# Kernel tuning notes

Hardware: AMD Instinct MI355X
Metric: run time of the kernel (lower is better)

The kernel has to match this reference:

```python
import jax, jax.numpy as jnp
import numpy as np

B, N, D, H = 2, 2048, 2048, 16
HD = D // H  # 128


def _rope(x, freqs):
    # x: [b,h,n,d]; freqs: [n, d//2] angles. Interleaved complex rotation.
    cos = jnp.cos(freqs)  # [n, d/2]
    sin = jnp.sin(freqs)
    x2 = x.reshape(*x.shape[:-1], -1, 2)  # [b,h,n,d/2,2]
    xr, xi = x2[..., 0], x2[..., 1]
    out_r = xr * cos - xi * sin
    out_i = xr * sin + xi * cos
    return jnp.stack([out_r, out_i], axis=-1).reshape(x.shape)


def setup_inputs() -> dict:
    key = jax.random.key(0)
    ks = jax.random.split(key, 4)
    x = jax.random.normal(ks[0], (B, N, D), jnp.float32)
    # rotary angle tables: pos * inv_freq, shape [N, HD/2]
    pos = jnp.arange(N, dtype=jnp.float32)
    inv_freq = 1.0 / (10000.0 ** (jnp.arange(0, HD, 2, dtype=jnp.float32) / HD))
    freqs = pos[:, None] * inv_freq[None, :]
    expanded_attn_masks = jnp.ones((B, 1, 1, N), jnp.int32)
    casual_mask = jnp.tril(jnp.ones((N, N), jnp.int32))[None, None]  # [1,1,N,N]
    Wqkv = jax.random.normal(ks[1], (D, 3 * D), jnp.float32) * 0.02
    bqkv = jnp.zeros((3 * D,), jnp.float32)
    Wout = jax.random.normal(ks[2], (D, D), jnp.float32) * 0.02
    bout = jnp.zeros((D,), jnp.float32)
    return {
        'x': x, 'freq_cis_q': freqs, 'freq_cis_k': freqs,
        'expanded_attn_masks': expanded_attn_masks, 'casual_mask': casual_mask,
        'Wqkv': Wqkv, 'bqkv': bqkv, 'Wout': Wout, 'bout': bout,
    }


def reference(x, freq_cis_q, freq_cis_k, expanded_attn_masks, casual_mask, Wqkv, bqkv, Wout, bout):
    b, n, d = x.shape
    qkv = x @ Wqkv + bqkv                                   # [b,n,3d]
    qkv = qkv.reshape(b, n, 3, H, HD)
    qkv = jnp.transpose(qkv, (2, 0, 3, 1, 4))               # c b h n d
    q, k, v = qkv[0], qkv[1], qkv[2]
    next_prefix_kv = jnp.stack((k, v))                      # pre-RoPE k cached, per source
    q = _rope(q, freq_cis_q)
    k = _rope(k, freq_cis_k)
    scores = jnp.einsum('bhqd,bhkd->bhqk', q, k) / jnp.sqrt(jnp.float32(HD))
    mask_value = -jnp.finfo(scores.dtype).max
    scores = jnp.where(casual_mask == 0, mask_value, scores)
    scores = jnp.where(expanded_attn_masks == 0, mask_value, scores)
    p = jax.nn.softmax(scores, axis=-1)                     # dropout_prob=0 -> identity
    attn_o = jnp.einsum('bhqk,bhkd->bhqd', p, v)
    attn_o = jnp.transpose(attn_o, (0, 2, 1, 3)).reshape(b, n, d)
    out = attn_o @ Wout + bout
    return out, next_prefix_kv
```

## Files before the change

kernel.cpp:

```cpp
#include <hip/hip_runtime.h>
#include <hip/hip_bf16.h>
#include <math.h>

#define B_ 2
#define N_ 2048
#define D_ 2048
#define H_ 16
#define HD_ 128
#define D3_ 6144

typedef __attribute__((ext_vector_type(8))) short bf16x8;
typedef __attribute__((ext_vector_type(4))) float f32x4;

__device__ __forceinline__ void gl_lds16(const void* g, void* l) {
  __builtin_amdgcn_global_load_lds(
      (const __attribute__((address_space(1))) void*)g,
      (__attribute__((address_space(3))) void*)l, 16, 0, 0);
}

__device__ __forceinline__ float bf2f(short s) {
  union { float f; unsigned u; } cv;
  cv.u = ((unsigned)(unsigned short)s) << 16;
  return cv.f;
}
__device__ __forceinline__ short f2bf(float f) {
  union { float f; unsigned u; } cv; cv.f = f;
  unsigned u = cv.u;
  unsigned r = (u + 0x7fffu + ((u >> 16) & 1u)) >> 16;
  return (short)r;
}

__global__ void k_cvt_x(const float* __restrict__ x, short* __restrict__ xb, int n) {
  int i = (blockIdx.x * 256 + threadIdx.x) * 4;
  if (i < n) {
    float4 v = *(const float4*)(x + i);
    short4 o;
    o.x = f2bf(v.x); o.y = f2bf(v.y); o.z = f2bf(v.z); o.w = f2bf(v.w);
    *(short4*)(xb + i) = o;
  }
}

__global__ void k_transcvt(const float* __restrict__ in, short* __restrict__ out, int R, int C) {
  __shared__ float t[64][65];
  int r0 = blockIdx.y * 64, c0 = blockIdx.x * 64;
  #pragma unroll
  for (int e0 = 0; e0 < 16; e0++) {
    int e = e0 * 256 + threadIdx.x;
    int r = e >> 6, c = e & 63;
    t[r][c] = in[(long)(r0 + r) * C + c0 + c];
  }
  __syncthreads();
  #pragma unroll
  for (int e0 = 0; e0 < 16; e0++) {
    int e = e0 * 256 + threadIdx.x;
    int c = e >> 6, r = e & 63;
    out[(long)(c0 + c) * R + r0 + r] = f2bf(t[r][c]);
  }
}

__global__ __launch_bounds__(256) void k_gemm(
    const short* __restrict__ A, const short* __restrict__ BT,
    const float* __restrict__ bias, int M, int Nn, int K, int mode,
    short* __restrict__ outb, float* __restrict__ outf, float* __restrict__ kvout)
{
  __shared__ __align__(16) short As[128 * 32];
  __shared__ __align__(16) short Bs[128 * 32];
  int wave = threadIdx.x >> 6, lane = threadIdx.x & 63;
  int quad = lane >> 4, l15 = lane & 15;
  int m0 = blockIdx.y * 128, n0 = blockIdx.x * 128;
  int wm = wave >> 1, wn = wave & 1;
  f32x4 acc[4][4] = {};

  for (int k0 = 0; k0 < K; k0 += 32) {
    const short* gaa = A + (long)(m0 + wave * 32 + (lane >> 2)) * K + k0 + (lane & 3) * 8;
    gl_lds16(gaa,           As + (wave * 32) * 32);
    gl_lds16(gaa + 16 * K,  As + (wave * 32 + 16) * 32);
    const short* gbb = BT + (long)(n0 + wave * 32 + (lane >> 2)) * K + k0 + (lane & 3) * 8;
    gl_lds16(gbb,           Bs + (wave * 32) * 32);
    gl_lds16(gbb + 16 * K,  Bs + (wave * 32 + 16) * 32);
    __syncthreads();
    bf16x8 af[4], bfr[4];
    #pragma unroll
    for (int mi = 0; mi < 4; mi++)
      af[mi] = *(const bf16x8*)(As + (wm * 64 + mi * 16 + l15) * 32 + quad * 8);
    #pragma unroll
    for (int ni = 0; ni < 4; ni++)
      bfr[ni] = *(const bf16x8*)(Bs + (wn * 64 + ni * 16 + l15) * 32 + quad * 8);
    #pragma unroll
    for (int mi = 0; mi < 4; mi++)
      #pragma unroll
      for (int ni = 0; ni < 4; ni++)
        acc[mi][ni] = __builtin_amdgcn_mfma_f32_16x16x32_bf16(af[mi], bfr[ni], acc[mi][ni], 0, 0, 0);
    __syncthreads();
  }

  int row_base = m0 + wm * 64;
  int col_base = n0 + wn * 64;
  #pragma unroll
  for (int mi = 0; mi < 4; mi++) {
    #pragma unroll
    for (int ni = 0; ni < 4; ni++) {
      int col = col_base + ni * 16 + l15;
      float bv = bias[col];
      #pragma unroll
      for (int reg = 0; reg < 4; reg++) {
        int row = row_base + mi * 16 + quad * 4 + reg;
        float v = acc[mi][ni][reg] + bv;
        if (mode == 0) {
          outf[(long)row * Nn + col] = v;
        } else {
          outb[(long)row * Nn + col] = f2bf(v);
          if (col >= D_) {
            int sel = (col >= 2 * D_) ? 1 : 0;
            int c2 = col - D_ - sel * D_;
            int h = c2 >> 7, d = c2 & 127;
            int b = row >> 11, n = row & 2047;
            kvout[((((long)sel * B_ + b) * H_ + h) * N_ + n) * HD_ + d] = v;
          }
        }
      }
    }
  }
}

__global__ void k_rope(const short* __restrict__ qkvb, const float* __restrict__ fq,
                       const float* __restrict__ fk, short* __restrict__ qr,
                       short* __restrict__ kr)
{
  int t = blockIdx.x * 256 + threadIdx.x;
  int i = t & 63;
  int n = (t >> 6) & (N_ - 1);
  int bh = t >> 17;
  int b = bh >> 4, h = bh & 15;
  long qrow = ((long)b * N_ + n) * D3_;
  float q0 = bf2f(qkvb[qrow + h * 128 + 2 * i]);
  float q1 = bf2f(qkvb[qrow + h * 128 + 2 * i + 1]);
  float k0 = bf2f(qkvb[qrow + D_ + h * 128 + 2 * i]);
  float k1 = bf2f(qkvb[qrow + D_ + h * 128 + 2 * i + 1]);
  float aq = fq[n * 64 + i], ak = fk[n * 64 + i];
  float cq, sq, ck, sk;
  __sincosf(aq, &sq, &cq);
  __sincosf(ak, &sk, &ck);
  const float qs = 0.08838834764831845f;
  long orow = ((long)bh * N_ + n) * HD_;
  qr[orow + 2 * i]     = f2bf((q0 * cq - q1 * sq) * qs);
  qr[orow + 2 * i + 1] = f2bf((q0 * sq + q1 * cq) * qs);
  kr[orow + 2 * i]     = f2bf(k0 * ck - k1 * sk);
  kr[orow + 2 * i + 1] = f2bf(k0 * sk + k1 * ck);
}

__global__ void k_vtrans(const short* __restrict__ qkvb, short* __restrict__ vt) {
  __shared__ short t[64][130];
  int nt = blockIdx.x & 31;
  int h = (blockIdx.x >> 5) & 15;
  int b = blockIdx.x >> 9;
  int n0 = nt * 64;
  #pragma unroll
  for (int e0 = 0; e0 < 32; e0++) {
    int e = e0 * 256 + threadIdx.x;
    int r = e >> 7, d = e & 127;
    t[r][d] = qkvb[((long)b * N_ + n0 + r) * D3_ + 2 * D_ + h * 128 + d];
  }
  __syncthreads();
  #pragma unroll
  for (int e0 = 0; e0 < 32; e0++) {
    int e = e0 * 256 + threadIdx.x;
    int d = e >> 6, r = e & 63;
    vt[(((long)(b * H_ + h)) * HD_ + d) * N_ + n0 + r] = t[r][d];
  }
}

__global__ __launch_bounds__(256) void k_flash(
    const short* __restrict__ qr, const short* __restrict__ kr,
    const short* __restrict__ vt, const int* __restrict__ amask,
    short* __restrict__ ao)
{
  __shared__ __align__(16) short Qs[64 * 128];
  __shared__ __align__(16) short Ks[64 * 128];
  __shared__ __align__(16) short Vs[128 * 64];
  __shared__ __align__(16) short Ps[4][16 * 64];
  int qt = blockIdx.x & 31, h = (blockIdx.x >> 5) & 15, b = blockIdx.x >> 9;
  int wave = threadIdx.x >> 6, lane = threadIdx.x & 63;
  int quad = lane >> 4, l15 = lane & 15;
  int q0 = qt * 64;
  long bh = (long)b * H_ + h;

  #pragma unroll
  for (int c = 0; c < 4; c++) {
    const short* g = qr + (bh * N_ + q0 + wave * 16 + c * 4 + (lane >> 4)) * HD_ + l15 * 8;
    gl_lds16(g, Qs + (wave * 16 + c * 4) * 128);
  }
  __syncthreads();
  bf16x8 aq[4];
  #pragma unroll
  for (int kt = 0; kt < 4; kt++)
    aq[kt] = *(const bf16x8*)(Qs + (wave * 16 + l15) * 128 + kt * 32 + quad * 8);

  f32x4 o[8] = {};
  float mrow[4] = {-3e38f, -3e38f, -3e38f, -3e38f};
  float lrow[4] = {0.f, 0.f, 0.f, 0.f};
  int rowq[4];
  #pragma unroll
  for (int reg = 0; reg < 4; reg++) rowq[reg] = q0 + wave * 16 + quad * 4 + reg;

  for (int kvt = 0; kvt <= qt; kvt++) {
    int kv0 = kvt * 64;
    __syncthreads();
    #pragma unroll
    for (int c = 0; c < 4; c++) {
      const short* g = kr + (bh * N_ + kv0 + wave * 16 + c * 4 + (lane >> 4)) * HD_ + l15 * 8;
      gl_lds16(g, Ks + (wave * 16 + c * 4) * 128);
    }
    #pragma unroll
    for (int c = 0; c < 4; c++) {
      const short* g = vt + (bh * HD_ + wave * 32 + c * 8 + (lane >> 3)) * N_ + kv0 + (lane & 7) * 8;
      gl_lds16(g, Vs + (wave * 32 + c * 8) * 64);
    }
    __syncthreads();

    f32x4 s[4] = {};
    #pragma unroll
    for (int kt = 0; kt < 4; kt++) {
      #pragma unroll
      for (int nt = 0; nt < 4; nt++) {
        bf16x8 bk = *(const bf16x8*)(Ks + (nt * 16 + l15) * 128 + kt * 32 + quad * 8);
        s[nt] = __builtin_amdgcn_mfma_f32_16x16x32_bf16(aq[kt], bk, s[nt], 0, 0, 0);
      }
    }
    #pragma unroll
    for (int nt = 0; nt < 4; nt++) {
      int col = kv0 + nt * 16 + l15;
      bool cm = (amask[b * N_ + col] == 0);
      #pragma unroll
      for (int reg = 0; reg < 4; reg++) {
        if (cm || col > rowq[reg]) s[nt][reg] = -3e38f;
      }
    }
    float mn[4], alpha[4];
    #pragma unroll
    for (int reg = 0; reg < 4; reg++) {
      float pm = fmaxf(fmaxf(s[0][reg], s[1][reg]), fmaxf(s[2][reg], s[3][reg]));
      #pragma unroll
      for (int x = 1; x < 16; x <<= 1) pm = fmaxf(pm, __shfl_xor(pm, x, 64));
      mn[reg] = fmaxf(mrow[reg], pm);
      alpha[reg] = __expf(mrow[reg] - mn[reg]);
      mrow[reg] = mn[reg];
    }
    float rs[4] = {0.f, 0.f, 0.f, 0.f};
    #pragma unroll
    for (int nt = 0; nt < 4; nt++)
      #pragma unroll
      for (int reg = 0; reg < 4; reg++) {
        float p = __expf(s[nt][reg] - mn[reg]);
        s[nt][reg] = p;
        rs[reg] += p;
      }
    #pragma unroll
    for (int reg = 0; reg < 4; reg++) {
      #pragma unroll
      for (int x = 1; x < 16; x <<= 1) rs[reg] += __shfl_xor(rs[reg], x, 64);
      lrow[reg] = lrow[reg] * alpha[reg] + rs[reg];
    }
    short* pw = Ps[wave];
    #pragma unroll
    for (int nt = 0; nt < 4; nt++)
      #pragma unroll
      for (int reg = 0; reg < 4; reg++)
        pw[(quad * 4 + reg) * 64 + nt * 16 + l15] = f2bf(s[nt][reg]);
    #pragma unroll
    for (int nt2 = 0; nt2 < 8; nt2++)
      #pragma unroll
      for (int reg = 0; reg < 4; reg++)
        o[nt2][reg] *= alpha[reg];
    asm volatile("s_waitcnt lgkmcnt(0)" ::: "memory");
    #pragma unroll
    for (int kt2 = 0; kt2 < 2; kt2++) {
      bf16x8 ap = *(const bf16x8*)(pw + l15 * 64 + kt2 * 32 + quad * 8);
      #pragma unroll
      for (int nt2 = 0; nt2 < 8; nt2++) {
        bf16x8 bv = *(const bf16x8*)(Vs + (nt2 * 16 + l15) * 64 + kt2 * 32 + quad * 8);
        o[nt2] = __builtin_amdgcn_mfma_f32_16x16x32_bf16(ap, bv, o[nt2], 0, 0, 0);
      }
    }
  }

  #pragma unroll
  for (int reg = 0; reg < 4; reg++) lrow[reg] = 1.0f / lrow[reg];
  #pragma unroll
  for (int nt2 = 0; nt2 < 8; nt2++)
    #pragma unroll
    for (int reg = 0; reg < 4; reg++) {
      int n = q0 + wave * 16 + quad * 4 + reg;
      int d = h * 128 + nt2 * 16 + l15;
      ao[((long)b * N_ + n) * D_ + d] = f2bf(o[nt2][reg] * lrow[reg]);
    }
}

extern "C" void kernel_launch(void* const* d_in, const int* in_sizes, int n_in,
                              void* d_out, int out_size, void* d_ws, size_t ws_size,
                              hipStream_t stream) {
  const float* x    = (const float*)d_in[0];
  const float* fq   = (const float*)d_in[1];
  const float* fk   = (const float*)d_in[2];
  const int*   am   = (const int*)d_in[3];
  const float* Wqkv = (const float*)d_in[5];
  const float* bqkv = (const float*)d_in[6];
  const float* Wout = (const float*)d_in[7];
  const float* bout = (const float*)d_in[8];

  float* out = (float*)d_out;
  float* kvout = out + (long)B_ * N_ * D_;

  char* ws = (char*)d_ws;
  const size_t need = 167772160;
  if (ws_size < need) return;
  short* xb    = (short*)(ws);
  short* wqkvT = (short*)(ws + 16777216);
  short* woutT = (short*)(ws + 41943040);
  short* qkvb  = (short*)(ws + 50331648);
  short* qrb   = (short*)(ws + 100663296);
  short* krb   = (short*)(ws + 117440512);
  short* vtb   = (short*)(ws + 134217728);
  short* aob   = (short*)(ws + 150994944);

  k_cvt_x<<<8192, 256, 0, stream>>>(x, xb, B_ * N_ * D_);
  k_transcvt<<<dim3(D3_ / 64, D_ / 64), 256, 0, stream>>>(Wqkv, wqkvT, D_, D3_);
  k_transcvt<<<dim3(D_ / 64, D_ / 64), 256, 0, stream>>>(Wout, woutT, D_, D_);
  k_gemm<<<dim3(D3_ / 128, (B_ * N_) / 128), 256, 0, stream>>>(
      xb, wqkvT, bqkv, B_ * N_, D3_, D_, 1, qkvb, nullptr, kvout);
  k_rope<<<16384, 256, 0, stream>>>(qkvb, fq, fk, qrb, krb);
  k_vtrans<<<1024, 256, 0, stream>>>(qkvb, vtb);
  k_flash<<<1024, 256, 0, stream>>>(qrb, krb, vtb, am, aob);
  k_gemm<<<dim3(D_ / 128, (B_ * N_) / 128), 256, 0, stream>>>(
      aob, woutT, bout, B_ * N_, D_, D_, 0, nullptr, out, nullptr);
}
```

Before: 688.5 us.

## Pair causal query tiles per block and swizzle LDS layouts in flash attention

Each flash-attention block now handles two query tiles, p and 31-p, so every block does the same amount of causal work. The two tiles share each K/V tile loaded into LDS, which halves the K/V global traffic. The Q, K and V LDS layouts get an XOR swizzle, and the P scratch rows are padded to 72 elements, to cut LDS bank conflicts. In exchange there are half as many blocks, and register pressure is higher because each wave keeps two sets of accumulators and Q fragments, which may lower occupancy.

```diff
diff --git a/kernel.cpp b/kernel.cpp
--- a/kernel.cpp
+++ b/kernel.cpp
@@ -175,124 +175,149 @@
     const short* __restrict__ vt, const int* __restrict__ amask,
     short* __restrict__ ao)
 {
-  __shared__ __align__(16) short Qs[64 * 128];
+  __shared__ __align__(16) short QsA[64 * 128];
+  __shared__ __align__(16) short QsB[64 * 128];
   __shared__ __align__(16) short Ks[64 * 128];
   __shared__ __align__(16) short Vs[128 * 64];
-  __shared__ __align__(16) short Ps[4][16 * 64];
-  int qt = blockIdx.x & 31, h = (blockIdx.x >> 5) & 15, b = blockIdx.x >> 9;
+  __shared__ __align__(16) short Ps[4][16 * 72];
+  int p = blockIdx.x & 15, bhidx = blockIdx.x >> 4;
+  int b = bhidx >> 4, h = bhidx & 15;
+  int qa = p, qb = 31 - p;
   int wave = threadIdx.x >> 6, lane = threadIdx.x & 63;
   int quad = lane >> 4, l15 = lane & 15;
-  int q0 = qt * 64;
   long bh = (long)b * H_ + h;
+  int q0A = qa * 64, q0B = qb * 64;
 
   #pragma unroll
   for (int c = 0; c < 4; c++) {
-    const short* g = qr + (bh * N_ + q0 + wave * 16 + c * 4 + (lane >> 4)) * HD_ + l15 * 8;
-    gl_lds16(g, Qs + (wave * 16 + c * 4) * 128);
+    int rl = wave * 16 + c * 4 + (lane >> 4);
+    int gc = (lane & 15) ^ (rl & 7);
+    gl_lds16(qr + (bh * N_ + q0A + rl) * HD_ + gc * 8, QsA + (wave * 16 + c * 4) * 128);
+    gl_lds16(qr + (bh * N_ + q0B + rl) * HD_ + gc * 8, QsB + (wave * 16 + c * 4) * 128);
   }
   __syncthreads();
-  bf16x8 aq[4];
-  #pragma unroll
-  for (int kt = 0; kt < 4; kt++)
-    aq[kt] = *(const bf16x8*)(Qs + (wave * 16 + l15) * 128 + kt * 32 + quad * 8);
-
-  f32x4 o[8] = {};
-  float mrow[4] = {-3e38f, -3e38f, -3e38f, -3e38f};
-  float lrow[4] = {0.f, 0.f, 0.f, 0.f};
-  int rowq[4];
-  #pragma unroll
-  for (int reg = 0; reg < 4; reg++) rowq[reg] = q0 + wave * 16 + quad * 4 + reg;
-
-  for (int kvt = 0; kvt <= qt; kvt++) {
+  bf16x8 aqA[4], aqB[4];
+  #pragma unroll
+  for (int kt = 0; kt < 4; kt++) {
+    int slot = (kt * 4 + quad) ^ (l15 & 7);
+    aqA[kt] = *(const bf16x8*)(QsA + (wave * 16 + l15) * 128 + slot * 8);
+    aqB[kt] = *(const bf16x8*)(QsB + (wave * 16 + l15) * 128 + slot * 8);
+  }
+
+  f32x4 oA[8] = {}, oB[8] = {};
+  float mA[4] = {-3e38f, -3e38f, -3e38f, -3e38f}, mB[4] = {-3e38f, -3e38f, -3e38f, -3e38f};
+  float lA[4] = {0.f, 0.f, 0.f, 0.f}, lB[4] = {0.f, 0.f, 0.f, 0.f};
+  int rowA[4], rowB[4];
+  #pragma unroll
+  for (int reg = 0; reg < 4; reg++) {
+    rowA[reg] = q0A + wave * 16 + quad * 4 + reg;
+    rowB[reg] = q0B + wave * 16 + quad * 4 + reg;
+  }
+  short* pw = Ps[wave];
+
+#define QSTEP(AQ, O, MR, LR, ROWQ)                                                     \
+  {                                                                                    \
+    f32x4 s[4] = {};                                                                   \
+    _Pragma("unroll")                                                                  \
+    for (int kt = 0; kt < 4; kt++) {                                                   \
+      _Pragma("unroll")                                                                \
+      for (int nt = 0; nt < 4; nt++) {                                                 \
+        int slot = (kt * 4 + quad) ^ (l15 & 7);                                        \
+        bf16x8 bk = *(const bf16x8*)(Ks + (nt * 16 + l15) * 128 + slot * 8);           \
+        s[nt] = __builtin_amdgcn_mfma_f32_16x16x32_bf16(AQ[kt], bk, s[nt], 0, 0, 0);   \
+      }                                                                                \
+    }                                                                                  \
+    _Pragma("unroll")                                                                  \
+    for (int nt = 0; nt < 4; nt++) {                                                   \
+      int col = kv0 + nt * 16 + l15;                                                   \
+      bool cm = (amask[b * N_ + col] == 0);                                            \
+      _Pragma("unroll")                                                                \
+      for (int reg = 0; reg < 4; reg++)                                                \
+        if (cm || col > ROWQ[reg]) s[nt][reg] = -3e38f;                                \
+    }                                                                                  \
+    float mn[4], alpha[4];                                                             \
+    _Pragma("unroll")                                                                  \
+    for (int reg = 0; reg < 4; reg++) {                                                \
+      float pm = fmaxf(fmaxf(s[0][reg], s[1][reg]), fmaxf(s[2][reg], s[3][reg]));      \
+      _Pragma("unroll")                                                                \
+      for (int x = 1; x < 16; x <<= 1) pm = fmaxf(pm, __shfl_xor(pm, x, 64));          \
+      mn[reg] = fmaxf(MR[reg], pm);                                                    \
+      alpha[reg] = __expf(MR[reg] - mn[reg]);                                          \
+      MR[reg] = mn[reg];                                                               \
+    }                                                                                  \
+    float rs[4] = {0.f, 0.f, 0.f, 0.f};                                                \
+    _Pragma("unroll")                                                                  \
+    for (int nt = 0; nt < 4; nt++)                                                     \
+      _Pragma("unroll")                                                                \
+      for (int reg = 0; reg < 4; reg++) {                                              \
+        float pp = __expf(s[nt][reg] - mn[reg]);                                       \
+        s[nt][reg] = pp;                                                               \
+        rs[reg] += pp;                                                                 \
+      }                                                                                \
+    _Pragma("unroll")                                                                  \
+    for (int reg = 0; reg < 4; reg++) {                                                \
+      _Pragma("unroll")                                                                \
+      for (int x = 1; x < 16; x <<= 1) rs[reg] += __shfl_xor(rs[reg], x, 64);          \
+      LR[reg] = LR[reg] * alpha[reg] + rs[reg];                                        \
+    }                                                                                  \
+    _Pragma("unroll")                                                                  \
+    for (int nt = 0; nt < 4; nt++)                                                     \
+      _Pragma("unroll")                                                                \
+      for (int reg = 0; reg < 4; reg++)                                                \
+        pw[(quad * 4 + reg) * 72 + nt * 16 + l15] = f2bf(s[nt][reg]);                  \
+    _Pragma("unroll")                                                                  \
+    for (int nt2 = 0; nt2 < 8; nt2++)                                                  \
+      _Pragma("unroll")                                                                \
+      for (int reg = 0; reg < 4; reg++)                                                \
+        O[nt2][reg] *= alpha[reg];                                                     \
+    asm volatile("s_waitcnt lgkmcnt(0)" ::: "memory");                                 \
+    _Pragma("unroll")                                                                  \
+    for (int kt2 = 0; kt2 < 2; kt2++) {                                                \
+      bf16x8 ap = *(const bf16x8*)(pw + l15 * 72 + kt2 * 32 + quad * 8);               \
+      _Pragma("unroll")                                                                \
+      for (int nt2 = 0; nt2 < 8; nt2++) {                                              \
+        int slot2 = (kt2 * 4 + quad) ^ (l15 & 7);                                      \
+        bf16x8 bv = *(const bf16x8*)(Vs + (nt2 * 16 + l15) * 64 + slot2 * 8);          \
+        O[nt2] = __builtin_amdgcn_mfma_f32_16x16x32_bf16(ap, bv, O[nt2], 0, 0, 0);     \
+      }                                                                                \
+    }                                                                                  \
+  }
+
+  for (int kvt = 0; kvt <= qb; kvt++) {
     int kv0 = kvt * 64;
     __syncthreads();
     #pragma unroll
     for (int c = 0; c < 4; c++) {
-      const short* g = kr + (bh * N_ + kv0 + wave * 16 + c * 4 + (lane >> 4)) * HD_ + l15 * 8;
-      gl_lds16(g, Ks + (wave * 16 + c * 4) * 128);
+      int rl = wave * 16 + c * 4 + (lane >> 4);
+      int gc = (lane & 15) ^ (rl & 7);
+      gl_lds16(kr + (bh * N_ + kv0 + rl) * HD_ + gc * 8, Ks + (wave * 16 + c * 4) * 128);
     }
     #pragma unroll
     for (int c = 0; c < 4; c++) {
-      const short* g = vt + (bh * HD_ + wave * 32 + c * 8 + (lane >> 3)) * N_ + kv0 + (lane & 7) * 8;
-      gl_lds16(g, Vs + (wave * 32 + c * 8) * 64);
+      int rl = wave * 32 + c * 8 + (lane >> 3);
+      int gc = (lane & 7) ^ (rl & 7);
+      gl_lds16(vt + (bh * HD_ + rl) * N_ + kv0 + gc * 8, Vs + (wave * 32 + c * 8) * 64);
     }
     __syncthreads();
 
-    f32x4 s[4] = {};
-    #pragma unroll
-    for (int kt = 0; kt < 4; kt++) {
-      #pragma unroll
-      for (int nt = 0; nt < 4; nt++) {
-        bf16x8 bk = *(const bf16x8*)(Ks + (nt * 16 + l15) * 128 + kt * 32 + quad * 8);
-        s[nt] = __builtin_amdgcn_mfma_f32_16x16x32_bf16(aq[kt], bk, s[nt], 0, 0, 0);
-      }
-    }
-    #pragma unroll
-    for (int nt = 0; nt < 4; nt++) {
-      int col = kv0 + nt * 16 + l15;
-      bool cm = (amask[b * N_ + col] == 0);
-      #pragma unroll
-      for (int reg = 0; reg < 4; reg++) {
-        if (cm || col > rowq[reg]) s[nt][reg] = -3e38f;
-      }
-    }
-    float mn[4], alpha[4];
+    QSTEP(aqB, oB, mB, lB, rowB);
+    if (kvt <= qa) {
+      QSTEP(aqA, oA, mA, lA, rowA);
+    }
+  }
+#undef QSTEP
+
+  #pragma unroll
+  for (int reg = 0; reg < 4; reg++) { lA[reg] = 1.0f / lA[reg]; lB[reg] = 1.0f / lB[reg]; }
+  #pragma unroll
+  for (int nt2 = 0; nt2 < 8; nt2++)
     #pragma unroll
     for (int reg = 0; reg < 4; reg++) {
-      float pm = fmaxf(fmaxf(s[0][reg], s[1][reg]), fmaxf(s[2][reg], s[3][reg]));
-      #pragma unroll
-      for (int x = 1; x < 16; x <<= 1) pm = fmaxf(pm, __shfl_xor(pm, x, 64));
-      mn[reg] = fmaxf(mrow[reg], pm);
-      alpha[reg] = __expf(mrow[reg] - mn[reg]);
-      mrow[reg] = mn[reg];
-    }
-    float rs[4] = {0.f, 0.f, 0.f, 0.f};
-    #pragma unroll
-    for (int nt = 0; nt < 4; nt++)
-      #pragma unroll
-      for (int reg = 0; reg < 4; reg++) {
-        float p = __expf(s[nt][reg] - mn[reg]);
-        s[nt][reg] = p;
-        rs[reg] += p;
-      }
-    #pragma unroll
-    for (int reg = 0; reg < 4; reg++) {
-      #pragma unroll
-      for (int x = 1; x < 16; x <<= 1) rs[reg] += __shfl_xor(rs[reg], x, 64);
-      lrow[reg] = lrow[reg] * alpha[reg] + rs[reg];
-    }
-    short* pw = Ps[wave];
-    #pragma unroll
-    for (int nt = 0; nt < 4; nt++)
-      #pragma unroll
-      for (int reg = 0; reg < 4; reg++)
-        pw[(quad * 4 + reg) * 64 + nt * 16 + l15] = f2bf(s[nt][reg]);
-    #pragma unroll
-    for (int nt2 = 0; nt2 < 8; nt2++)
-      #pragma unroll
-      for (int reg = 0; reg < 4; reg++)
-        o[nt2][reg] *= alpha[reg];
-    asm volatile("s_waitcnt lgkmcnt(0)" ::: "memory");
-    #pragma unroll
-    for (int kt2 = 0; kt2 < 2; kt2++) {
-      bf16x8 ap = *(const bf16x8*)(pw + l15 * 64 + kt2 * 32 + quad * 8);
-      #pragma unroll
-      for (int nt2 = 0; nt2 < 8; nt2++) {
-        bf16x8 bv = *(const bf16x8*)(Vs + (nt2 * 16 + l15) * 64 + kt2 * 32 + quad * 8);
-        o[nt2] = __builtin_amdgcn_mfma_f32_16x16x32_bf16(ap, bv, o[nt2], 0, 0, 0);
-      }
-    }
-  }
-
-  #pragma unroll
-  for (int reg = 0; reg < 4; reg++) lrow[reg] = 1.0f / lrow[reg];
-  #pragma unroll
-  for (int nt2 = 0; nt2 < 8; nt2++)
-    #pragma unroll
-    for (int reg = 0; reg < 4; reg++) {
-      int n = q0 + wave * 16 + quad * 4 + reg;
       int d = h * 128 + nt2 * 16 + l15;
-      ao[((long)b * N_ + n) * D_ + d] = f2bf(o[nt2][reg] * lrow[reg]);
+      int nA = q0A + wave * 16 + quad * 4 + reg;
+      int nB = q0B + wave * 16 + quad * 4 + reg;
+      ao[((long)b * N_ + nA) * D_ + d] = f2bf(oA[nt2][reg] * lA[reg]);
+      ao[((long)b * N_ + nB) * D_ + d] = f2bf(oB[nt2][reg] * lB[reg]);
     }
 }
 
@@ -330,7 +355,7 @@
       xb, wqkvT, bqkv, B_ * N_, D3_, D_, 1, qkvb, nullptr, kvout);
   k_rope<<<16384, 256, 0, stream>>>(qkvb, fq, fk, qrb, krb);
   k_vtrans<<<1024, 256, 0, stream>>>(qkvb, vtb);
-  k_flash<<<1024, 256, 0, stream>>>(qrb, krb, vtb, am, aob);
+  k_flash<<<512, 256, 0, stream>>>(qrb, krb, vtb, am, aob);
   k_gemm<<<dim3(D_ / 128, (B_ * N_) / 128), 256, 0, stream>>>(
       aob, woutT, bout, B_ * N_, D_, D_, 0, nullptr, out, nullptr);
 }
```

Result: faster. 557.2 us (-19.1%).
